# Optimization experiments

Measured on AMD Instinct MI355X. Metric: run time of the kernel, lower is better.

The kernel has to match this reference:

```python
import jax, jax.numpy as jnp
import numpy as np

B, S, N = 32, 64, 8192


def setup_inputs() -> dict:
    key = jax.random.key(0)
    k1, k2 = jax.random.split(key)
    x = jax.random.normal(k1, (B, S, N), dtype=jnp.float32)
    xref = jax.random.normal(k2, (B, S, N), dtype=jnp.float32)
    return {"x": x, "xref": xref}


def reference(x, xref):
    # Batched circular cross-correlation via FFT: corr = ifft(conj(fft(x)) * fft(xref)).real
    x32 = x.astype(jnp.float32)
    xref32 = xref.astype(jnp.float32)
    x_fft = jnp.fft.fft(x32, axis=-1)            # [B,S,N] complex64
    xref_fft = jnp.fft.fft(xref32, axis=-1)
    corr = jnp.real(jnp.fft.ifft(jnp.conj(x_fft) * xref_fft, axis=-1))  # [B,S,N]
    ind = jnp.argmax(corr, axis=-1)              # [B,S] int32
    n = x.shape[-1]
    # torch.roll(x, ind): out[k] = x[(k - ind) mod N]; vectorized circular shift via gather
    pos = (jnp.arange(n)[None, None, :] - ind[..., None]) % n  # [B,S,N]
    x_aligned = jnp.take_along_axis(x32, pos, axis=-1)
    inds = ind.astype(jnp.float32)               # original stores into a float zeros tensor
    return (x_aligned, inds)
```

## Files before the change

kernel.cpp:

```cpp
#include <hip/hip_runtime.h>
#include <hip/hip_bf16.h>

#define NFFT 8192
#define TPB  512
#define VPT  16

typedef float f2 __attribute__((ext_vector_type(2)));

__device__ __forceinline__ f2 mk(float a, float b){ f2 r; r.x=a; r.y=b; return r; }
__device__ __forceinline__ f2 cswap(f2 a){ return __builtin_shufflevector(a,a,1,0); }

__device__ __forceinline__ int swz(int j) { return j ^ ((j >> 4) & 15); }
__device__ __forceinline__ int rev13(unsigned x) { return (int)(__brev(x) >> 19); }

__device__ __forceinline__ f2 cmul_conj(f2 d, float c, float s){
  return d*c + cswap(d)*mk(s,-s);
}
__device__ __forceinline__ f2 cmul_pos(f2 v, float c, float s){
  return v*c + cswap(v)*mk(-s,s);
}

template<int S>
__device__ __forceinline__ void make_tw(int p, float* cA, float* sA,
                                        float* cB, float* sB, float& c4, float& s4) {
  float r = (float)p * (0.125f / (float)S);
  float sa = __builtin_amdgcn_sinf(r);
  float ca = __builtin_amdgcn_cosf(r);
  float c2 = ca*ca - sa*sa, s2 = 2.0f*ca*sa;
  c4 = c2*c2 - s2*s2; s4 = 2.0f*c2*s2;
  const float R = 0.70710678118654752f;
  cA[0] = ca;          sA[0] = sa;
  cA[1] = R*(ca-sa);   sA[1] = R*(ca+sa);
  cA[2] = -sa;         sA[2] = ca;
  cA[3] = -R*(ca+sa);  sA[3] = R*(ca-sa);
  cB[0] = c2;  sB[0] = s2;
  cB[1] = -s2; sB[1] = c2;
}

template<int S>
__device__ __forceinline__ void dif_round(f2* z, int t) {
  #pragma unroll
  for (int gi = 0; gi < 2; ++gi) {
    int g = t + TPB*gi;
    int p = g & (S-1);
    int blk = g / S;
    int base = blk*(8*S) + p;
    f2 y[8];
    #pragma unroll
    for (int k = 0; k < 8; ++k) y[k] = z[swz(base + k*S)];
    float cA[4], sA[4], cB[2], sB[2], c4, s4;
    make_tw<S>(p, cA, sA, cB, sB, c4, s4);
    #pragma unroll
    for (int k = 0; k < 4; ++k) {
      f2 u = y[k], v = y[k+4];
      y[k] = u + v;
      y[k+4] = cmul_conj(u - v, cA[k], sA[k]);
    }
    #pragma unroll
    for (int h = 0; h < 8; h += 4)
      #pragma unroll
      for (int k0 = 0; k0 < 2; ++k0) {
        f2 u = y[h+k0], v = y[h+k0+2];
        y[h+k0] = u + v;
        y[h+k0+2] = cmul_conj(u - v, cB[k0], sB[k0]);
      }
    #pragma unroll
    for (int h = 0; h < 8; h += 2) {
      f2 u = y[h], v = y[h+1];
      y[h] = u + v;
      y[h+1] = cmul_conj(u - v, c4, s4);
    }
    #pragma unroll
    for (int k = 0; k < 8; ++k) z[swz(base + k*S)] = y[k];
  }
  __syncthreads();
}

template<int S>
__device__ __forceinline__ void dit_round(f2* z, int t) {
  #pragma unroll
  for (int gi = 0; gi < 2; ++gi) {
    int g = t + TPB*gi;
    int p = g & (S-1);
    int blk = g / S;
    int base = blk*(8*S) + p;
    f2 y[8];
    #pragma unroll
    for (int k = 0; k < 8; ++k) y[k] = z[swz(base + k*S)];
    float cA[4], sA[4], cB[2], sB[2], c4, s4;
    make_tw<S>(p, cA, sA, cB, sB, c4, s4);
    #pragma unroll
    for (int h = 0; h < 8; h += 2) {
      f2 u = y[h];
      f2 w = cmul_pos(y[h+1], c4, s4);
      y[h] = u + w; y[h+1] = u - w;
    }
    #pragma unroll
    for (int h = 0; h < 8; h += 4)
      #pragma unroll
      for (int k0 = 0; k0 < 2; ++k0) {
        f2 u = y[h+k0];
        f2 w = cmul_pos(y[h+k0+2], cB[k0], sB[k0]);
        y[h+k0] = u + w; y[h+k0+2] = u - w;
      }
    #pragma unroll
    for (int k = 0; k < 4; ++k) {
      f2 u = y[k];
      f2 w = cmul_pos(y[k+4], cA[k], sA[k]);
      y[k] = u + w; y[k+4] = u - w;
    }
    #pragma unroll
    for (int k = 0; k < 8; ++k) z[swz(base + k*S)] = y[k];
  }
  __syncthreads();
}

#define C16_1 0.92387953251128674f
#define S16_1 0.38268343236508978f
#define RSQ2  0.70710678118654752f

__device__ __forceinline__ void dif16(f2* z, int t) {
  const float C8[8] = {1.f, C16_1, RSQ2, S16_1, 0.f, -S16_1, -RSQ2, -C16_1};
  const float S8[8] = {0.f, S16_1, RSQ2, C16_1, 1.f,  C16_1,  RSQ2,  S16_1};
  f2 y[16];
  int base = 16*t;
  #pragma unroll
  for (int k = 0; k < 16; ++k) y[k] = z[swz(base+k)];
  #pragma unroll
  for (int j = 0; j < 8; ++j) {
    f2 u = y[j], v = y[j+8];
    y[j] = u + v;
    y[j+8] = cmul_conj(u - v, C8[j], S8[j]);
  }
  #pragma unroll
  for (int h = 0; h < 16; h += 8)
    #pragma unroll
    for (int j = 0; j < 4; ++j) {
      f2 u = y[h+j], v = y[h+j+4];
      y[h+j] = u + v;
      y[h+j+4] = cmul_conj(u - v, C8[2*j], S8[2*j]);
    }
  #pragma unroll
  for (int h = 0; h < 16; h += 4)
    #pragma unroll
    for (int j = 0; j < 2; ++j) {
      f2 u = y[h+j], v = y[h+j+2];
      y[h+j] = u + v;
      f2 d = u - v;
      y[h+j+2] = j ? mk(d.y, -d.x) : d;
    }
  #pragma unroll
  for (int h = 0; h < 16; h += 2) {
    f2 u = y[h], v = y[h+1];
    y[h] = u + v; y[h+1] = u - v;
  }
  #pragma unroll
  for (int k = 0; k < 16; ++k) z[swz(base+k)] = y[k];
  __syncthreads();
}

__device__ __forceinline__ void dit16(f2* z, int t) {
  const float C8[8] = {1.f, C16_1, RSQ2, S16_1, 0.f, -S16_1, -RSQ2, -C16_1};
  const float S8[8] = {0.f, S16_1, RSQ2, C16_1, 1.f,  C16_1,  RSQ2,  S16_1};
  f2 y[16];
  int base = 16*t;
  #pragma unroll
  for (int k = 0; k < 16; ++k) y[k] = z[swz(base+k)];
  #pragma unroll
  for (int h = 0; h < 16; h += 2) {
    f2 u = y[h], w = y[h+1];
    y[h] = u + w; y[h+1] = u - w;
  }
  #pragma unroll
  for (int h = 0; h < 16; h += 4)
    #pragma unroll
    for (int j = 0; j < 2; ++j) {
      f2 u = y[h+j];
      f2 v = y[h+j+2];
      f2 w = j ? mk(-v.y, v.x) : v;
      y[h+j] = u + w; y[h+j+2] = u - w;
    }
  #pragma unroll
  for (int h = 0; h < 16; h += 8)
    #pragma unroll
    for (int j = 0; j < 4; ++j) {
      f2 u = y[h+j];
      f2 w = cmul_pos(y[h+j+4], C8[2*j], S8[2*j]);
      y[h+j] = u + w; y[h+j+4] = u - w;
    }
  #pragma unroll
  for (int j = 0; j < 8; ++j) {
    f2 u = y[j];
    f2 w = cmul_pos(y[j+8], C8[j], S8[j]);
    y[j] = u + w; y[j+8] = u - w;
  }
  #pragma unroll
  for (int k = 0; k < 16; ++k) z[swz(base+k)] = y[k];
  __syncthreads();
}

__device__ __forceinline__ void dit_last(const f2* z, int t, float* re, float& mv) {
  #pragma unroll
  for (int gi = 0; gi < 2; ++gi) {
    const int S = 1024;
    int g = t + TPB*gi;
    int base = g;
    f2 y[8];
    #pragma unroll
    for (int k = 0; k < 8; ++k) y[k] = z[swz(base + k*S)];
    float cA[4], sA[4], cB[2], sB[2], c4, s4;
    make_tw<S>(g, cA, sA, cB, sB, c4, s4);
    #pragma unroll
    for (int h = 0; h < 8; h += 2) {
      f2 u = y[h];
      f2 w = cmul_pos(y[h+1], c4, s4);
      y[h] = u + w; y[h+1] = u - w;
    }
    #pragma unroll
    for (int h = 0; h < 8; h += 4)
      #pragma unroll
      for (int k0 = 0; k0 < 2; ++k0) {
        f2 u = y[h+k0];
        f2 w = cmul_pos(y[h+k0+2], cB[k0], sB[k0]);
        y[h+k0] = u + w; y[h+k0+2] = u - w;
      }
    #pragma unroll
    for (int k = 0; k < 4; ++k) {
      f2 u = y[k];
      f2 w = cmul_pos(y[k+4], cA[k], sA[k]);
      y[k] = u + w; y[k+4] = u - w;
    }
    #pragma unroll
    for (int k = 0; k < 8; ++k) {
      re[8*gi + k] = y[k].x;
      mv = fmaxf(mv, y[k].x);
    }
  }
}

__global__ __launch_bounds__(TPB)
void corr_align_kernel(const float* __restrict__ x, const float* __restrict__ xref,
                       float* __restrict__ out0, float* __restrict__ outInd) {
  __shared__ f2 z[NFFT];
  const int t = threadIdx.x;
  const int row = blockIdx.x;
  const float* xrow = x + (size_t)row * NFFT;
  const float* rrow = xref + (size_t)row * NFFT;

  const float4* x4 = (const float4*)xrow;
  const float4* r4 = (const float4*)rrow;
  #pragma unroll
  for (int gi = 0; gi < 4; ++gi) {
    int q = t + TPB*gi;
    float4 xv = x4[q], rv = r4[q];
    int j = 4*q;
    z[swz(j+0)] = mk(xv.x, rv.x);
    z[swz(j+1)] = mk(xv.y, rv.y);
    z[swz(j+2)] = mk(xv.z, rv.z);
    z[swz(j+3)] = mk(xv.w, rv.w);
  }
  __syncthreads();

  dif_round<1024>(z, t);
  dif_round<128>(z, t);
  dif_round<16>(z, t);
  dif16(z, t);

  #pragma unroll
  for (int gi = 0; gi < 8; ++gi) {
    int k = 8*t + gi + 1;
    int p = rev13((unsigned)k);
    int q = rev13((unsigned)((NFFT - k) & (NFFT-1)));
    f2 Zp = z[swz(p)];
    f2 Zq = z[swz(q)];
    float Xx = 0.5f*(Zp.x + Zq.x);
    float Xy = 0.5f*(Zp.y - Zq.y);
    float Yx = 0.5f*(Zp.y + Zq.y);
    float Yy = 0.5f*(Zq.x - Zp.x);
    f2 Gk = mk(Xx*Yx + Xy*Yy, Xx*Yy - Xy*Yx);
    z[swz(p)] = Gk;
    if (k != NFFT/2) z[swz(q)] = mk(Gk.x, -Gk.y);
  }
  if (t == 0) {
    f2 Z0 = z[0];
    z[0] = mk(Z0.x * Z0.y, 0.0f);
  }
  __syncthreads();

  dit16(z, t);
  dit_round<16>(z, t);
  dit_round<128>(z, t);
  float re[16];
  float mv = -3.0e38f;
  dit_last(z, t, re, mv);
  __syncthreads();

  float* zf = (float*)z;
  int*  zi = (int*)z;
  if (t == 0) zi[8] = 0;
  #pragma unroll
  for (int off = 32; off > 0; off >>= 1)
    mv = fmaxf(mv, __shfl_down(mv, off));
  const int lane = t & 63, wave = t >> 6;
  if (lane == 0) zf[wave] = mv;
  __syncthreads();
  float M = zf[0];
  #pragma unroll
  for (int w = 1; w < 8; ++w) M = fmaxf(M, zf[w]);
  float thresh = M - 32768.0f;
  #pragma unroll
  for (int gi = 0; gi < 2; ++gi)
    #pragma unroll
    for (int k = 0; k < 8; ++k) {
      if (re[8*gi + k] >= thresh) {
        int pos = t + TPB*gi + 1024*k;
        int slot = atomicAdd(&zi[8], 1);
        if (slot < 40) zi[16 + slot] = pos;
      }
    }
  __syncthreads();
  int count = zi[8];
  if (count > 40) count = 40;

  int bestPos;
  if (count == 1) {
    bestPos = zi[16];
  } else {
    double* zd = (double*)z;
    double bestV = -1.0e300;
    int bp = NFFT;
    for (int c = 0; c < count; ++c) {
      int pos = zi[16 + c];
      double part = 0.0;
      #pragma unroll 4
      for (int gi = 0; gi < VPT; ++gi) {
        int n = t + TPB*gi;
        part += (double)xrow[n] * (double)rrow[(n + pos) & (NFFT-1)];
      }
      #pragma unroll
      for (int off = 32; off > 0; off >>= 1)
        part += __shfl_down(part, off);
      if (lane == 0) zd[32 + wave] = part;
      __syncthreads();
      if (t == 0) {
        double tot = 0.0;
        #pragma unroll
        for (int w = 0; w < 8; ++w) tot += zd[32 + w];
        if (tot > bestV || (tot == bestV && pos < bp)) { bestV = tot; bp = pos; }
      }
      __syncthreads();
    }
    if (t == 0) zi[9] = bp;
    __syncthreads();
    bestPos = zi[9];
  }

  float* orow = out0 + (size_t)row * NFFT;
  #pragma unroll 4
  for (int gi = 0; gi < VPT; ++gi) {
    int kk = t + TPB*gi;
    orow[kk] = xrow[(kk - bestPos) & (NFFT-1)];
  }
  if (t == 0) outInd[row] = (float)bestPos;
}

extern "C" void kernel_launch(void* const* d_in, const int* in_sizes, int n_in,
                              void* d_out, int out_size, void* d_ws, size_t ws_size,
                              hipStream_t stream) {
  const float* x    = (const float*)d_in[0];
  const float* xref = (const float*)d_in[1];
  float* out = (float*)d_out;
  const int rows = in_sizes[0] / NFFT;
  float* outInd = out + (size_t)rows * NFFT;
  hipLaunchKernelGGL(corr_align_kernel, dim3(rows), dim3(TPB), 0, stream,
                     x, xref, out, outInd);
}
```

Measured before the change: 234.7 us.

## Remap inner FFT stages per wavefront to replace block barriers with wave fences

After the first radix-8 stride-1024 stage, each 1024-point sub-FFT is assigned to a single wavefront. The inner radix-8 and radix-16 stages on both the forward and inverse paths then synchronise only with an LDS waitcnt fence instead of __syncthreads. This cuts the number of workgroup-wide barriers per FFT pass. It relies on wave-synchronous execution and on the inline-asm fence ordering LDS traffic correctly within a wave, which is a correctness risk if the compiler reorders accesses.

```diff
diff --git a/kernel.cpp b/kernel.cpp
--- a/kernel.cpp
+++ b/kernel.cpp
@@ -4,6 +4,8 @@
 #define NFFT 8192
 #define TPB  512
 #define VPT  16
+
+#define WAVE_FENCE() asm volatile("s_waitcnt lgkmcnt(0)" ::: "memory")
 
 typedef float f2 __attribute__((ext_vector_type(2)));
 
@@ -37,93 +39,139 @@
   cB[1] = -s2; sB[1] = c2;
 }
 
+__device__ __forceinline__ void dif8_core(f2* y, int p_num, float inv_den) {
+  float cA[4], sA[4], cB[2], sB[2], c4, s4;
+  {
+    float r = (float)p_num * inv_den;
+    float sa = __builtin_amdgcn_sinf(r);
+    float ca = __builtin_amdgcn_cosf(r);
+    float c2 = ca*ca - sa*sa, s2 = 2.0f*ca*sa;
+    c4 = c2*c2 - s2*s2; s4 = 2.0f*c2*s2;
+    const float R = 0.70710678118654752f;
+    cA[0] = ca;          sA[0] = sa;
+    cA[1] = R*(ca-sa);   sA[1] = R*(ca+sa);
+    cA[2] = -sa;         sA[2] = ca;
+    cA[3] = -R*(ca+sa);  sA[3] = R*(ca-sa);
+    cB[0] = c2;  sB[0] = s2;
+    cB[1] = -s2; sB[1] = c2;
+  }
+  #pragma unroll
+  for (int k = 0; k < 4; ++k) {
+    f2 u = y[k], v = y[k+4];
+    y[k] = u + v;
+    y[k+4] = cmul_conj(u - v, cA[k], sA[k]);
+  }
+  #pragma unroll
+  for (int h = 0; h < 8; h += 4)
+    #pragma unroll
+    for (int k0 = 0; k0 < 2; ++k0) {
+      f2 u = y[h+k0], v = y[h+k0+2];
+      y[h+k0] = u + v;
+      y[h+k0+2] = cmul_conj(u - v, cB[k0], sB[k0]);
+    }
+  #pragma unroll
+  for (int h = 0; h < 8; h += 2) {
+    f2 u = y[h], v = y[h+1];
+    y[h] = u + v;
+    y[h+1] = cmul_conj(u - v, c4, s4);
+  }
+}
+
+__device__ __forceinline__ void dit8_core(f2* y, int p_num, float inv_den) {
+  float cA[4], sA[4], cB[2], sB[2], c4, s4;
+  {
+    float r = (float)p_num * inv_den;
+    float sa = __builtin_amdgcn_sinf(r);
+    float ca = __builtin_amdgcn_cosf(r);
+    float c2 = ca*ca - sa*sa, s2 = 2.0f*ca*sa;
+    c4 = c2*c2 - s2*s2; s4 = 2.0f*c2*s2;
+    const float R = 0.70710678118654752f;
+    cA[0] = ca;          sA[0] = sa;
+    cA[1] = R*(ca-sa);   sA[1] = R*(ca+sa);
+    cA[2] = -sa;         sA[2] = ca;
+    cA[3] = -R*(ca+sa);  sA[3] = R*(ca-sa);
+    cB[0] = c2;  sB[0] = s2;
+    cB[1] = -s2; sB[1] = c2;
+  }
+  #pragma unroll
+  for (int h = 0; h < 8; h += 2) {
+    f2 u = y[h];
+    f2 w = cmul_pos(y[h+1], c4, s4);
+    y[h] = u + w; y[h+1] = u - w;
+  }
+  #pragma unroll
+  for (int h = 0; h < 8; h += 4)
+    #pragma unroll
+    for (int k0 = 0; k0 < 2; ++k0) {
+      f2 u = y[h+k0];
+      f2 w = cmul_pos(y[h+k0+2], cB[k0], sB[k0]);
+      y[h+k0] = u + w; y[h+k0+2] = u - w;
+    }
+  #pragma unroll
+  for (int k = 0; k < 4; ++k) {
+    f2 u = y[k];
+    f2 w = cmul_pos(y[k+4], cA[k], sA[k]);
+    y[k] = u + w; y[k+4] = u - w;
+  }
+}
+
+__device__ __forceinline__ void dif_global1024(f2* z, int t) {
+  #pragma unroll
+  for (int gi = 0; gi < 2; ++gi) {
+    int p = t + TPB*gi;
+    f2 y[8];
+    #pragma unroll
+    for (int k = 0; k < 8; ++k) y[k] = z[swz(p + k*1024)];
+    dif8_core(y, p, 0.125f/1024.0f);
+    #pragma unroll
+    for (int k = 0; k < 8; ++k) z[swz(p + k*1024)] = y[k];
+  }
+  __syncthreads();
+}
+
 template<int S>
-__device__ __forceinline__ void dif_round(f2* z, int t) {
+__device__ __forceinline__ void dif_wave(f2* z, int w, int l) {
   #pragma unroll
   for (int gi = 0; gi < 2; ++gi) {
-    int g = t + TPB*gi;
-    int p = g & (S-1);
-    int blk = g / S;
-    int base = blk*(8*S) + p;
+    int gl = l + 64*gi;
+    int p = gl & (S-1);
+    int base = w*1024 + (gl/S)*(8*S) + p;
     f2 y[8];
     #pragma unroll
     for (int k = 0; k < 8; ++k) y[k] = z[swz(base + k*S)];
-    float cA[4], sA[4], cB[2], sB[2], c4, s4;
-    make_tw<S>(p, cA, sA, cB, sB, c4, s4);
-    #pragma unroll
-    for (int k = 0; k < 4; ++k) {
-      f2 u = y[k], v = y[k+4];
-      y[k] = u + v;
-      y[k+4] = cmul_conj(u - v, cA[k], sA[k]);
-    }
-    #pragma unroll
-    for (int h = 0; h < 8; h += 4)
-      #pragma unroll
-      for (int k0 = 0; k0 < 2; ++k0) {
-        f2 u = y[h+k0], v = y[h+k0+2];
-        y[h+k0] = u + v;
-        y[h+k0+2] = cmul_conj(u - v, cB[k0], sB[k0]);
-      }
-    #pragma unroll
-    for (int h = 0; h < 8; h += 2) {
-      f2 u = y[h], v = y[h+1];
-      y[h] = u + v;
-      y[h+1] = cmul_conj(u - v, c4, s4);
-    }
+    dif8_core(y, p, 0.125f/(float)S);
     #pragma unroll
     for (int k = 0; k < 8; ++k) z[swz(base + k*S)] = y[k];
   }
-  __syncthreads();
+  WAVE_FENCE();
 }
 
 template<int S>
-__device__ __forceinline__ void dit_round(f2* z, int t) {
+__device__ __forceinline__ void dit_wave(f2* z, int w, int l) {
   #pragma unroll
   for (int gi = 0; gi < 2; ++gi) {
-    int g = t + TPB*gi;
-    int p = g & (S-1);
-    int blk = g / S;
-    int base = blk*(8*S) + p;
+    int gl = l + 64*gi;
+    int p = gl & (S-1);
+    int base = w*1024 + (gl/S)*(8*S) + p;
     f2 y[8];
     #pragma unroll
     for (int k = 0; k < 8; ++k) y[k] = z[swz(base + k*S)];
-    float cA[4], sA[4], cB[2], sB[2], c4, s4;
-    make_tw<S>(p, cA, sA, cB, sB, c4, s4);
-    #pragma unroll
-    for (int h = 0; h < 8; h += 2) {
-      f2 u = y[h];
-      f2 w = cmul_pos(y[h+1], c4, s4);
-      y[h] = u + w; y[h+1] = u - w;
-    }
-    #pragma unroll
-    for (int h = 0; h < 8; h += 4)
-      #pragma unroll
-      for (int k0 = 0; k0 < 2; ++k0) {
-        f2 u = y[h+k0];
-        f2 w = cmul_pos(y[h+k0+2], cB[k0], sB[k0]);
-        y[h+k0] = u + w; y[h+k0+2] = u - w;
-      }
-    #pragma unroll
-    for (int k = 0; k < 4; ++k) {
-      f2 u = y[k];
-      f2 w = cmul_pos(y[k+4], cA[k], sA[k]);
-      y[k] = u + w; y[k+4] = u - w;
-    }
+    dit8_core(y, p, 0.125f/(float)S);
     #pragma unroll
     for (int k = 0; k < 8; ++k) z[swz(base + k*S)] = y[k];
   }
-  __syncthreads();
+  WAVE_FENCE();
 }
 
 #define C16_1 0.92387953251128674f
 #define S16_1 0.38268343236508978f
 #define RSQ2  0.70710678118654752f
 
-__device__ __forceinline__ void dif16(f2* z, int t) {
+__device__ __forceinline__ void dif16_wave(f2* z, int w, int l) {
   const float C8[8] = {1.f, C16_1, RSQ2, S16_1, 0.f, -S16_1, -RSQ2, -C16_1};
   const float S8[8] = {0.f, S16_1, RSQ2, C16_1, 1.f,  C16_1,  RSQ2,  S16_1};
   f2 y[16];
-  int base = 16*t;
+  int base = w*1024 + 16*l;
   #pragma unroll
   for (int k = 0; k < 16; ++k) y[k] = z[swz(base+k)];
   #pragma unroll
@@ -156,20 +204,20 @@
   }
   #pragma unroll
   for (int k = 0; k < 16; ++k) z[swz(base+k)] = y[k];
-  __syncthreads();
-}
-
-__device__ __forceinline__ void dit16(f2* z, int t) {
+  WAVE_FENCE();
+}
+
+__device__ __forceinline__ void dit16_wave(f2* z, int w, int l) {
   const float C8[8] = {1.f, C16_1, RSQ2, S16_1, 0.f, -S16_1, -RSQ2, -C16_1};
   const float S8[8] = {0.f, S16_1, RSQ2, C16_1, 1.f,  C16_1,  RSQ2,  S16_1};
   f2 y[16];
-  int base = 16*t;
+  int base = w*1024 + 16*l;
   #pragma unroll
   for (int k = 0; k < 16; ++k) y[k] = z[swz(base+k)];
   #pragma unroll
   for (int h = 0; h < 16; h += 2) {
-    f2 u = y[h], w = y[h+1];
-    y[h] = u + w; y[h+1] = u - w;
+    f2 u = y[h], v = y[h+1];
+    y[h] = u + v; y[h+1] = u - v;
   }
   #pragma unroll
   for (int h = 0; h < 16; h += 4)
@@ -177,59 +225,36 @@
     for (int j = 0; j < 2; ++j) {
       f2 u = y[h+j];
       f2 v = y[h+j+2];
-      f2 w = j ? mk(-v.y, v.x) : v;
-      y[h+j] = u + w; y[h+j+2] = u - w;
+      f2 ww = j ? mk(-v.y, v.x) : v;
+      y[h+j] = u + ww; y[h+j+2] = u - ww;
     }
   #pragma unroll
   for (int h = 0; h < 16; h += 8)
     #pragma unroll
     for (int j = 0; j < 4; ++j) {
       f2 u = y[h+j];
-      f2 w = cmul_pos(y[h+j+4], C8[2*j], S8[2*j]);
-      y[h+j] = u + w; y[h+j+4] = u - w;
+      f2 ww = cmul_pos(y[h+j+4], C8[2*j], S8[2*j]);
+      y[h+j] = u + ww; y[h+j+4] = u - ww;
     }
   #pragma unroll
   for (int j = 0; j < 8; ++j) {
     f2 u = y[j];
-    f2 w = cmul_pos(y[j+8], C8[j], S8[j]);
-    y[j] = u + w; y[j+8] = u - w;
+    f2 ww = cmul_pos(y[j+8], C8[j], S8[j]);
+    y[j] = u + ww; y[j+8] = u - ww;
   }
   #pragma unroll
   for (int k = 0; k < 16; ++k) z[swz(base+k)] = y[k];
-  __syncthreads();
+  WAVE_FENCE();
 }
 
 __device__ __forceinline__ void dit_last(const f2* z, int t, float* re, float& mv) {
   #pragma unroll
   for (int gi = 0; gi < 2; ++gi) {
-    const int S = 1024;
     int g = t + TPB*gi;
-    int base = g;
     f2 y[8];
     #pragma unroll
-    for (int k = 0; k < 8; ++k) y[k] = z[swz(base + k*S)];
-    float cA[4], sA[4], cB[2], sB[2], c4, s4;
-    make_tw<S>(g, cA, sA, cB, sB, c4, s4);
-    #pragma unroll
-    for (int h = 0; h < 8; h += 2) {
-      f2 u = y[h];
-      f2 w = cmul_pos(y[h+1], c4, s4);
-      y[h] = u + w; y[h+1] = u - w;
-    }
-    #pragma unroll
-    for (int h = 0; h < 8; h += 4)
-      #pragma unroll
-      for (int k0 = 0; k0 < 2; ++k0) {
-        f2 u = y[h+k0];
-        f2 w = cmul_pos(y[h+k0+2], cB[k0], sB[k0]);
-        y[h+k0] = u + w; y[h+k0+2] = u - w;
-      }
-    #pragma unroll
-    for (int k = 0; k < 4; ++k) {
-      f2 u = y[k];
-      f2 w = cmul_pos(y[k+4], cA[k], sA[k]);
-      y[k] = u + w; y[k+4] = u - w;
-    }
+    for (int k = 0; k < 8; ++k) y[k] = z[swz(g + k*1024)];
+    dit8_core(y, g, 0.125f/1024.0f);
     #pragma unroll
     for (int k = 0; k < 8; ++k) {
       re[8*gi + k] = y[k].x;
@@ -243,6 +268,7 @@
                        float* __restrict__ out0, float* __restrict__ outInd) {
   __shared__ f2 z[NFFT];
   const int t = threadIdx.x;
+  const int lane = t & 63, wave = t >> 6;
   const int row = blockIdx.x;
   const float* xrow = x + (size_t)row * NFFT;
   const float* rrow = xref + (size_t)row * NFFT;
@@ -261,10 +287,11 @@
   }
   __syncthreads();
 
-  dif_round<1024>(z, t);
-  dif_round<128>(z, t);
-  dif_round<16>(z, t);
-  dif16(z, t);
+  dif_global1024(z, t);
+  dif_wave<128>(z, wave, lane);
+  dif_wave<16>(z, wave, lane);
+  dif16_wave(z, wave, lane);
+  __syncthreads();
 
   #pragma unroll
   for (int gi = 0; gi < 8; ++gi) {
@@ -287,9 +314,10 @@
   }
   __syncthreads();
 
-  dit16(z, t);
-  dit_round<16>(z, t);
-  dit_round<128>(z, t);
+  dit16_wave(z, wave, lane);
+  dit_wave<16>(z, wave, lane);
+  dit_wave<128>(z, wave, lane);
+  __syncthreads();
   float re[16];
   float mv = -3.0e38f;
   dit_last(z, t, re, mv);
@@ -301,7 +329,6 @@
   #pragma unroll
   for (int off = 32; off > 0; off >>= 1)
     mv = fmaxf(mv, __shfl_down(mv, off));
-  const int lane = t & 63, wave = t >> 6;
   if (lane == 0) zf[wave] = mv;
   __syncthreads();
   float M = zf[0];
```

After: 234.0 us. No clear change (-0.3%).
